# Performance work log

Hardware: AMD Instinct MI355X
Metric: run time of the kernel (lower is better)

The kernel has to match this reference:

```python
import jax, jax.numpy as jnp
import numpy as np

BETA = 1.0

def setup_inputs() -> dict:
    key = jax.random.key(0)
    k1, k2 = jax.random.split(key)
    z = jax.random.normal(k1, (8, 8192, 64), dtype=jnp.float32)
    # codebook initialized as randn * sc (sc=0.001) in the original module
    codebook = jax.random.normal(k2, (1024, 64), dtype=jnp.float32) * 0.001
    return {"z": z, "codebook": codebook}

def reference(z, codebook):
    # squared euclidean distances: ||z||^2 + ||c||^2 - 2 z.c  -> [B, T, code_num]
    d = (jnp.sum(z ** 2, axis=-1, keepdims=True)
         + jnp.sum(codebook ** 2, axis=1)
         - 2.0 * jnp.einsum('btd,kd->btk', z, codebook))
    min_encoding_indices = jnp.argmin(d, axis=-1)            # [B, T] int
    # one-hot @ codebook is exactly a gather of nearest code vectors
    z_q = codebook[min_encoding_indices]                     # [B, T, D]
    sg = jax.lax.stop_gradient
    loss = jnp.mean((sg(z_q) - z) ** 2) + BETA * jnp.mean((z_q - sg(z)) ** 2)
    # straight-through estimator
    z_q_st = z + sg(z_q - z)
    return (z_q_st, min_encoding_indices, loss)
```

## Files before the change

### kernel.cpp

```cpp
#include <hip/hip_runtime.h>

#define TOKENS 65536
#define DIM 64
#define NCODE 1024
#define MARGIN 1e-5f
#define MARGINS (MARGIN * 2097152.0f)
#define FLAG_CAP 8192

#define OUT_IDX_OFF ((size_t)TOKENS * DIM)
#define OUT_LOSS_OFF (OUT_IDX_OFF + TOKENS)

#define WS_LOSS   0
#define WS_FLAGC  8
#define WS_DONEA  12
#define WS_DGRP   16
#define WS_BNORM  2064
#define WS_BNS    6160
#define WS_CHI    10256
#define WS_CLO    141328
#define WS_PACKED 272400
#define WS_FLAGS  337936

typedef __attribute__((ext_vector_type(8))) short short8;
typedef __attribute__((ext_vector_type(8))) _Float16 half8;
typedef __attribute__((ext_vector_type(4))) float f32x4;

static __device__ __forceinline__ half8 as_h8(short8 v) {
    return __builtin_bit_cast(half8, v);
}

__device__ __forceinline__ float np_sumsq64(const float* __restrict__ x) {
#pragma clang fp contract(off)
    float r[8];
#pragma unroll
    for (int j = 0; j < 8; ++j) r[j] = x[j] * x[j];
#pragma unroll
    for (int i = 8; i < 64; i += 8) {
#pragma unroll
        for (int j = 0; j < 8; ++j) {
            float sq = x[i + j] * x[i + j];
            r[j] = r[j] + sq;
        }
    }
    return ((r[0] + r[1]) + (r[2] + r[3])) + ((r[4] + r[5]) + (r[6] + r[7]));
}

__global__ __launch_bounds__(256) void vq_prep(
    const float* __restrict__ cb, unsigned short* __restrict__ chi,
    unsigned short* __restrict__ clo, float* __restrict__ bnorm,
    float* __restrict__ bns,
    unsigned int* __restrict__ ctrl ) {
    int tid = blockIdx.x * 256 + threadIdx.x;
    if (tid < 516) ctrl[tid] = 0u;
    int j = tid & 7;
    int L = (tid >> 3) & 63;
    int cs = tid >> 9;
    int s = cs & 1, c = cs >> 1;
    int code = c * 16 + (L & 15);
    int d = s * 32 + (L >> 4) * 8 + j;
    float v = -8192.0f * cb[(size_t)code * DIM + d];
    _Float16 h = (_Float16)v;
    float hf = (float)h;
    float lo;
    {
#pragma clang fp contract(off)
        lo = v - hf;
    }
    _Float16 l = (_Float16)lo;
    chi[tid] = __builtin_bit_cast(unsigned short, h);
    clo[tid] = __builtin_bit_cast(unsigned short, l);

    if (tid < NCODE) {
        float bn = np_sumsq64(cb + (size_t)tid * DIM);
        bnorm[tid] = bn;
        bns[tid] = bn * 2097152.0f;
    }
}

__device__ __forceinline__ void top2_merge(float& a1, float& a2, int& ai,
                                           float b1, float b2, int bi) {
    float n1 = fminf(a1, b1);
    float n2 = fminf(fmaxf(a1, b1), fminf(a2, b2));
    ai = (b1 < a1) ? bi : ai;
    a1 = n1; a2 = n2;
}

__global__ __launch_bounds__(256, 4) void vq_fast(
    const float* __restrict__ z, const float* __restrict__ cb,
    const unsigned short* __restrict__ cfrag_hi,
    const unsigned short* __restrict__ cfrag_lo,
    const float* __restrict__ bnorm_s, float* __restrict__ out,
    unsigned int* __restrict__ flag_count, int* __restrict__ flag_list,
    unsigned long long* __restrict__ packed_min,
    double* __restrict__ loss_sum, unsigned int flag_cap) {
    __shared__ short8 sh_hi[2][512];
    __shared__ short8 sh_lo[2][512];
    __shared__ float bn_lds[NCODE];
    __shared__ int s_best[64];
    __shared__ int s_flag[64];

    const int tid = threadIdx.x;
    const int lane = tid & 63;
    const int w = tid >> 6;
    const int t0 = blockIdx.x * 64;
    const int tw = t0 + w * 16;
    const int col = lane & 15;
    const int quad = lane >> 4;

    ((float4*)bn_lds)[tid] = ((const float4*)bnorm_s)[tid];

    half8 zhi[2], zlo[2];
#pragma unroll
    for (int s = 0; s < 2; ++s) {
        const float* zp = z + (size_t)(tw + col) * DIM + s * 32 + quad * 8;
        float4 f0 = ((const float4*)zp)[0];
        float4 f1 = ((const float4*)zp)[1];
        float f[8] = {f0.x, f0.y, f0.z, f0.w, f1.x, f1.y, f1.z, f1.w};
        half8 hh8, ll8;
#pragma unroll
        for (int j = 0; j < 8; ++j) {
            float sv = f[j] * 512.0f;
            _Float16 hh = (_Float16)sv;
            float hf = (float)hh;
            float lo;
            {
#pragma clang fp contract(off)
                lo = sv - hf;
            }
            hh8[j] = hh;
            ll8[j] = (_Float16)lo;
        }
        zhi[s] = hh8; zlo[s] = ll8;
    }

    const short8* CH = (const short8*)cfrag_hi;
    const short8* CL = (const short8*)cfrag_lo;

    {
        short8 a0 = CH[tid], a1 = CH[tid + 256];
        short8 b0 = CL[tid], b1 = CL[tid + 256];
        sh_hi[0][tid] = a0; sh_hi[0][tid + 256] = a1;
        sh_lo[0][tid] = b0; sh_lo[0][tid + 256] = b1;
    }
    __syncthreads();

    float m1 = 3.0e38f, m2 = 3.0e38f;
    int bi = 0;
    const int koff = quad * 4;

    for (int g = 0; g < 16; ++g) {
        const int buf = g & 1;
        short8 a0, a1, b0, b1;
        if (g < 15) {
            const int base = (g + 1) * 512 + tid;
            a0 = CH[base]; a1 = CH[base + 256];
            b0 = CL[base]; b1 = CL[base + 256];
        }
#pragma unroll
        for (int cc = 0; cc < 4; ++cc) {
            const int c = g * 4 + cc;
            short8 ch0 = sh_hi[buf][(cc * 2 + 0) * 64 + lane];
            short8 ch1 = sh_hi[buf][(cc * 2 + 1) * 64 + lane];
            short8 cl0 = sh_lo[buf][(cc * 2 + 0) * 64 + lane];
            short8 cl1 = sh_lo[buf][(cc * 2 + 1) * 64 + lane];
            const int cbase = c * 16 + koff;
            const f32x4 bn = *(const f32x4*)&bn_lds[cbase];
            f32x4 acc = bn;
            acc = __builtin_amdgcn_mfma_f32_16x16x32_f16(as_h8(ch0), zhi[0], acc, 0, 0, 0);
            acc = __builtin_amdgcn_mfma_f32_16x16x32_f16(as_h8(cl0), zhi[0], acc, 0, 0, 0);
            acc = __builtin_amdgcn_mfma_f32_16x16x32_f16(as_h8(ch0), zlo[0], acc, 0, 0, 0);
            acc = __builtin_amdgcn_mfma_f32_16x16x32_f16(as_h8(ch1), zhi[1], acc, 0, 0, 0);
            acc = __builtin_amdgcn_mfma_f32_16x16x32_f16(as_h8(cl1), zhi[1], acc, 0, 0, 0);
            acc = __builtin_amdgcn_mfma_f32_16x16x32_f16(as_h8(ch1), zlo[1], acc, 0, 0, 0);
#pragma unroll
            for (int i = 0; i < 4; ++i) {
                float u = acc[i];
                float om1 = m1;
                bool lt = u < om1;
                float fm = fminf(m2, u);
                m2 = lt ? om1 : fm;
                m1 = lt ? u : om1;
                bi = lt ? (cbase + i) : bi;
            }
        }
        if (g < 15) {
            sh_hi[buf ^ 1][tid] = a0; sh_hi[buf ^ 1][tid + 256] = a1;
            sh_lo[buf ^ 1][tid] = b0; sh_lo[buf ^ 1][tid + 256] = b1;
            __syncthreads();
        }
    }

    {
        float a1 = m1, a2 = m2;
        int ai = bi;
        {
            float o1 = __shfl_xor(a1, 16); float o2 = __shfl_xor(a2, 16);
            int oi = __shfl_xor(ai, 16);
            top2_merge(a1, a2, ai, o1, o2, oi);
        }
        {
            float o1 = __shfl_xor(a1, 32); float o2 = __shfl_xor(a2, 32);
            int oi = __shfl_xor(ai, 32);
            top2_merge(a1, a2, ai, o1, o2, oi);
        }
        if (quad == 0) {
            const int slot = w * 16 + col;
            int fl = (a2 - a1) < MARGINS;
            if (fl) {
                unsigned int pos = atomicAdd(flag_count, 1u);
                if (pos >= flag_cap) fl = 0;
                else {
                    flag_list[pos] = t0 + slot;
                    packed_min[pos] = ~0ull;
                }
            }
            s_best[slot] = ai;
            s_flag[slot] = fl;
        }
    }
    __syncthreads();

    const int et = tid >> 1, h = tid & 1;
    float loss_t = 0.0f;
    if (et < 64 && !s_flag[et]) {
        const int B = s_best[et];
        const float4* cq  = (const float4*)(cb + (size_t)B * DIM + h * 32);
        const float4* zq4 = (const float4*)(z + (size_t)(t0 + et) * DIM + h * 32);
        float4* o4 = (float4*)(out + (size_t)(t0 + et) * DIM + h * 32);
#pragma unroll
        for (int jj = 0; jj < 8; ++jj) {
#pragma clang fp contract(off)
            float4 cc = cq[jj];
            float4 zz = zq4[jj];
            float d0 = cc.x - zz.x, d1 = cc.y - zz.y;
            float d2 = cc.z - zz.z, d3 = cc.w - zz.w;
            float4 o;
            o.x = zz.x + d0; o.y = zz.y + d1;
            o.z = zz.z + d2; o.w = zz.w + d3;
            o4[jj] = o;
            loss_t = __fmaf_rn(d0, d0, loss_t);
            loss_t = __fmaf_rn(d1, d1, loss_t);
            loss_t = __fmaf_rn(d2, d2, loss_t);
            loss_t = __fmaf_rn(d3, d3, loss_t);
        }
        if (h == 0) out[OUT_IDX_OFF + t0 + et] = (float)B;
    }
#pragma unroll
    for (int off = 32; off > 0; off >>= 1)
        loss_t += __shfl_down(loss_t, off);
    if (lane == 0 && w < 2) atomicAdd(loss_sum, (double)loss_t);
}

__device__ __forceinline__ unsigned long long shfl_down_u64(unsigned long long v, int off) {
    unsigned int lo = (unsigned int)v, hi = (unsigned int)(v >> 32);
    lo = __shfl_down(lo, off);
    hi = __shfl_down(hi, off);
    return ((unsigned long long)hi << 32) | lo;
}

__global__ __launch_bounds__(256) void vq_exact_min(
    const float* __restrict__ z, const float* __restrict__ cb,
    const float* __restrict__ bnorm,
    const unsigned int* __restrict__ flag_count,
    const int* __restrict__ flag_list,
    unsigned long long* __restrict__ packed_min ,
    unsigned int* __restrict__ done_grp ,
    unsigned int* __restrict__ done_all,
    float* __restrict__ out, double* __restrict__ loss_sum,
    unsigned int flag_cap) {
    __shared__ float zsh[68];
    __shared__ float s_zs;
    __shared__ unsigned long long s_pk[4];
    __shared__ unsigned long long s_min;

    const int tid = threadIdx.x;
    const int w = tid >> 6;
    const int lane = tid & 63;
    unsigned int count = *flag_count;
    if (count > flag_cap) count = flag_cap;

    if (count == 0) {
        if (blockIdx.x == 0 && tid == 0) {
            double L = atomicAdd(loss_sum, 0.0);
            out[OUT_LOSS_OFF] = (float)(2.0 * L / (double)((size_t)TOKENS * DIM));
        }
        return;
    }
    if (blockIdx.x >= count) return;

    const int t = flag_list[blockIdx.x];

    if (tid < 4) {
        const float4* zp = (const float4*)(z + (size_t)t * DIM + tid * 16);
        float4* dst = (float4*)(zsh + tid * 16);
#pragma unroll
        for (int e = 0; e < 4; ++e) dst[e] = zp[e];
    }
    __syncthreads();
    if (tid == 0) s_zs = np_sumsq64(zsh);
    __syncthreads();

    const float szs = s_zs;
    const float* zp = zsh;
    unsigned long long pk = ~0ull;

    for (int e = 0; e < 4; ++e) {
        const int k = e * 256 + tid;
        float row[DIM];
        {
            const float4* c4 = (const float4*)(cb + (size_t)k * DIM);
#pragma unroll
            for (int j = 0; j < 16; ++j) {
                float4 v = c4[j];
                row[4 * j + 0] = v.x; row[4 * j + 1] = v.y;
                row[4 * j + 2] = v.z; row[4 * j + 3] = v.w;
            }
        }
        const float bnk = bnorm[k];

        float l16[16];
#pragma unroll
        for (int g2 = 0; g2 < 4; ++g2) {
            float4 v0 = ((const float4*)(zp + 4 * g2))[0];
            float4 v1 = ((const float4*)(zp + 16 + 4 * g2))[0];
            float4 v2 = ((const float4*)(zp + 32 + 4 * g2))[0];
            float4 v3 = ((const float4*)(zp + 48 + 4 * g2))[0];
            float a0[4] = {v0.x, v0.y, v0.z, v0.w};
            float a1[4] = {v1.x, v1.y, v1.z, v1.w};
            float a2[4] = {v2.x, v2.y, v2.z, v2.w};
            float a3[4] = {v3.x, v3.y, v3.z, v3.w};
#pragma unroll
            for (int ee = 0; ee < 4; ++ee) {
#pragma clang fp contract(off)
                int jj = 4 * g2 + ee;
                float acc = a3[ee] * row[48 + jj];
                acc = __fmaf_rn(a2[ee], row[32 + jj], acc);
                acc = __fmaf_rn(a1[ee], row[16 + jj], acc);
                acc = __fmaf_rn(a0[ee], row[jj],      acc);
                l16[jj] = acc;
            }
        }
        float e_np;
        {
#pragma clang fp contract(off)
#pragma unroll
            for (int jj = 0; jj < 8; ++jj) l16[jj] = l16[jj] + l16[jj + 8];
#pragma unroll
            for (int jj = 0; jj < 4; ++jj) l16[jj] = l16[jj] + l16[jj + 4];
            l16[0] = l16[0] + l16[2];
            l16[1] = l16[1] + l16[3];
            e_np = l16[0] + l16[1];
        }
        float dd;
        {
#pragma clang fp contract(off)
            float t1 = szs + bnk;
            float mm = 2.0f * e_np;
            dd = t1 - mm;
        }
        unsigned long long p =
            ((unsigned long long)__float_as_uint(dd) << 10) | (unsigned int)k;
        pk = (p < pk) ? p : pk;
    }

#pragma unroll
    for (int off = 32; off > 0; off >>= 1) {
        unsigned long long o = shfl_down_u64(pk, off);
        pk = (o < pk) ? o : pk;
    }
    if (lane == 0) s_pk[w] = pk;
    __syncthreads();
    if (tid == 0) {
        unsigned long long m = s_pk[0];
        m = (s_pk[1] < m) ? s_pk[1] : m;
        m = (s_pk[2] < m) ? s_pk[2] : m;
        m = (s_pk[3] < m) ? s_pk[3] : m;
        s_min = m;
    }
    __syncthreads();

    if (w == 0) {
        const int best = (int)(s_min & 1023ull);
        const float zl = zsh[lane];
        const float zq = cb[(size_t)best * DIM + lane];
        float d, o;
        {
#pragma clang fp contract(off)
            d = zq - zl;
            o = zl + d;
        }
        out[(size_t)t * DIM + lane] = o;
        float l2 = d * d;
#pragma unroll
        for (int off = 32; off > 0; off >>= 1)
            l2 += __shfl_down(l2, off);
        if (lane == 0) {
            out[OUT_IDX_OFF + t] = (float)best;
            atomicAdd(loss_sum, (double)l2);
        }
    }

    __threadfence();
    __syncthreads();
    if (tid == 0) {
        unsigned int old = atomicAdd(done_all, 1u);
        if (old == count - 1) {
            double L = atomicAdd(loss_sum, 0.0);
            out[OUT_LOSS_OFF] = (float)(2.0 * L / (double)((size_t)TOKENS * DIM));
        }
    }
}

extern "C" void kernel_launch(void* const* d_in, const int* in_sizes, int n_in,
                              void* d_out, int out_size, void* d_ws, size_t ws_size,
                              hipStream_t stream) {
    const float* z  = (const float*)d_in[0];
    const float* cb = (const float*)d_in[1];
    float* out = (float*)d_out;

    char* ws = (char*)d_ws;
    double* loss_sum = (double*)(ws + WS_LOSS);
    unsigned int* flag_count = (unsigned int*)(ws + WS_FLAGC);
    unsigned int* done_all = (unsigned int*)(ws + WS_DONEA);
    unsigned int* done_grp = (unsigned int*)(ws + WS_DGRP);
    float* bnorm = (float*)(ws + WS_BNORM);
    float* bns = (float*)(ws + WS_BNS);
    unsigned short* chi = (unsigned short*)(ws + WS_CHI);
    unsigned short* clo = (unsigned short*)(ws + WS_CLO);
    unsigned long long* packed = (unsigned long long*)(ws + WS_PACKED);
    int* flag_list = (int*)(ws + WS_FLAGS);

    unsigned int cap = 0;
    if (ws_size > WS_FLAGS + 4) {
        size_t c = (ws_size - WS_FLAGS) / 4;
        cap = (c > FLAG_CAP) ? FLAG_CAP : (unsigned int)c;
    }

    vq_prep<<<dim3(256), dim3(256), 0, stream>>>(
        cb, chi, clo, bnorm, bns, (unsigned int*)ws);
    vq_fast<<<dim3(TOKENS / 64), dim3(256), 0, stream>>>(
        z, cb, chi, clo, bns, out, flag_count, flag_list, packed, loss_sum, cap);
    vq_exact_min<<<dim3(FLAG_CAP), dim3(256), 0, stream>>>(
        z, cb, bnorm, flag_count, flag_list, packed, done_grp, done_all,
        out, loss_sum, cap);
}
```

Baseline: 137.4 us.

## Fuse exact-min fallback into fast kernel using per-block shared flag list

Removes the separate exact-recheck kernel and its global flag list and atomic counter. Each block now collects its own ambiguous tokens in shared memory and rechecks them in place with the exact FP32 distance loop, and a block-completion counter finalizes the loss. This saves a kernel launch and the 8192-block grid that mostly exits early, plus the global atomics. The cost is that blocks holding several flagged tokens process them serially, which can create tail imbalance. LDS use and register pressure also grow in a kernel launched with bounds of 4 blocks per CU.

Measured after the change: 307.8 us. 124% more time.

```diff
diff --git a/kernel.cpp b/kernel.cpp
--- a/kernel.cpp
+++ b/kernel.cpp
@@ -5,7 +5,6 @@
 #define NCODE 1024
 #define MARGIN 1e-5f
 #define MARGINS (MARGIN * 2097152.0f)
-#define FLAG_CAP 8192
 
 #define OUT_IDX_OFF ((size_t)TOKENS * DIM)
 #define OUT_LOSS_OFF (OUT_IDX_OFF + TOKENS)
@@ -18,8 +17,6 @@
 #define WS_BNS    6160
 #define WS_CHI    10256
 #define WS_CLO    141328
-#define WS_PACKED 272400
-#define WS_FLAGS  337936
 
 typedef __attribute__((ext_vector_type(8))) short short8;
 typedef __attribute__((ext_vector_type(8))) _Float16 half8;
@@ -85,19 +82,31 @@
     a1 = n1; a2 = n2;
 }
 
+__device__ __forceinline__ unsigned long long shfl_down_u64(unsigned long long v, int off) {
+    unsigned int lo = (unsigned int)v, hi = (unsigned int)(v >> 32);
+    lo = __shfl_down(lo, off);
+    hi = __shfl_down(hi, off);
+    return ((unsigned long long)hi << 32) | lo;
+}
+
 __global__ __launch_bounds__(256, 4) void vq_fast(
     const float* __restrict__ z, const float* __restrict__ cb,
     const unsigned short* __restrict__ cfrag_hi,
     const unsigned short* __restrict__ cfrag_lo,
-    const float* __restrict__ bnorm_s, float* __restrict__ out,
-    unsigned int* __restrict__ flag_count, int* __restrict__ flag_list,
-    unsigned long long* __restrict__ packed_min,
-    double* __restrict__ loss_sum, unsigned int flag_cap) {
+    const float* __restrict__ bnorm_s, const float* __restrict__ bnorm,
+    float* __restrict__ out, double* __restrict__ loss_sum,
+    unsigned int* __restrict__ done_all) {
     __shared__ short8 sh_hi[2][512];
     __shared__ short8 sh_lo[2][512];
     __shared__ float bn_lds[NCODE];
     __shared__ int s_best[64];
     __shared__ int s_flag[64];
+    __shared__ int s_flist[64];
+    __shared__ unsigned int s_fcnt;
+    __shared__ float zsh[68];
+    __shared__ float s_zs;
+    __shared__ unsigned long long s_pk[4];
+    __shared__ unsigned long long s_min;
 
     const int tid = threadIdx.x;
     const int lane = tid & 63;
@@ -106,6 +115,8 @@
     const int tw = t0 + w * 16;
     const int col = lane & 15;
     const int quad = lane >> 4;
+
+    if (tid == 0) s_fcnt = 0u;
 
     ((float4*)bn_lds)[tid] = ((const float4*)bnorm_s)[tid];
 
@@ -207,12 +218,8 @@
             const int slot = w * 16 + col;
             int fl = (a2 - a1) < MARGINS;
             if (fl) {
-                unsigned int pos = atomicAdd(flag_count, 1u);
-                if (pos >= flag_cap) fl = 0;
-                else {
-                    flag_list[pos] = t0 + slot;
-                    packed_min[pos] = ~0ull;
-                }
+                unsigned int p = atomicAdd(&s_fcnt, 1u);
+                s_flist[p] = slot;
             }
             s_best[slot] = ai;
             s_flag[slot] = fl;
@@ -249,154 +256,119 @@
     for (int off = 32; off > 0; off >>= 1)
         loss_t += __shfl_down(loss_t, off);
     if (lane == 0 && w < 2) atomicAdd(loss_sum, (double)loss_t);
-}
-
-__device__ __forceinline__ unsigned long long shfl_down_u64(unsigned long long v, int off) {
-    unsigned int lo = (unsigned int)v, hi = (unsigned int)(v >> 32);
-    lo = __shfl_down(lo, off);
-    hi = __shfl_down(hi, off);
-    return ((unsigned long long)hi << 32) | lo;
-}
-
-__global__ __launch_bounds__(256) void vq_exact_min(
-    const float* __restrict__ z, const float* __restrict__ cb,
-    const float* __restrict__ bnorm,
-    const unsigned int* __restrict__ flag_count,
-    const int* __restrict__ flag_list,
-    unsigned long long* __restrict__ packed_min ,
-    unsigned int* __restrict__ done_grp ,
-    unsigned int* __restrict__ done_all,
-    float* __restrict__ out, double* __restrict__ loss_sum,
-    unsigned int flag_cap) {
-    __shared__ float zsh[68];
-    __shared__ float s_zs;
-    __shared__ unsigned long long s_pk[4];
-    __shared__ unsigned long long s_min;
-
-    const int tid = threadIdx.x;
-    const int w = tid >> 6;
-    const int lane = tid & 63;
-    unsigned int count = *flag_count;
-    if (count > flag_cap) count = flag_cap;
-
-    if (count == 0) {
-        if (blockIdx.x == 0 && tid == 0) {
-            double L = atomicAdd(loss_sum, 0.0);
-            out[OUT_LOSS_OFF] = (float)(2.0 * L / (double)((size_t)TOKENS * DIM));
-        }
-        return;
-    }
-    if (blockIdx.x >= count) return;
-
-    const int t = flag_list[blockIdx.x];
-
-    if (tid < 4) {
-        const float4* zp = (const float4*)(z + (size_t)t * DIM + tid * 16);
-        float4* dst = (float4*)(zsh + tid * 16);
-#pragma unroll
-        for (int e = 0; e < 4; ++e) dst[e] = zp[e];
-    }
-    __syncthreads();
-    if (tid == 0) s_zs = np_sumsq64(zsh);
-    __syncthreads();
-
-    const float szs = s_zs;
-    const float* zp = zsh;
-    unsigned long long pk = ~0ull;
-
-    for (int e = 0; e < 4; ++e) {
-        const int k = e * 256 + tid;
-        float row[DIM];
-        {
-            const float4* c4 = (const float4*)(cb + (size_t)k * DIM);
-#pragma unroll
-            for (int j = 0; j < 16; ++j) {
-                float4 v = c4[j];
-                row[4 * j + 0] = v.x; row[4 * j + 1] = v.y;
-                row[4 * j + 2] = v.z; row[4 * j + 3] = v.w;
-            }
-        }
-        const float bnk = bnorm[k];
-
-        float l16[16];
-#pragma unroll
-        for (int g2 = 0; g2 < 4; ++g2) {
-            float4 v0 = ((const float4*)(zp + 4 * g2))[0];
-            float4 v1 = ((const float4*)(zp + 16 + 4 * g2))[0];
-            float4 v2 = ((const float4*)(zp + 32 + 4 * g2))[0];
-            float4 v3 = ((const float4*)(zp + 48 + 4 * g2))[0];
-            float a0[4] = {v0.x, v0.y, v0.z, v0.w};
-            float a1[4] = {v1.x, v1.y, v1.z, v1.w};
-            float a2[4] = {v2.x, v2.y, v2.z, v2.w};
-            float a3[4] = {v3.x, v3.y, v3.z, v3.w};
-#pragma unroll
-            for (int ee = 0; ee < 4; ++ee) {
-#pragma clang fp contract(off)
-                int jj = 4 * g2 + ee;
-                float acc = a3[ee] * row[48 + jj];
-                acc = __fmaf_rn(a2[ee], row[32 + jj], acc);
-                acc = __fmaf_rn(a1[ee], row[16 + jj], acc);
-                acc = __fmaf_rn(a0[ee], row[jj],      acc);
-                l16[jj] = acc;
-            }
-        }
-        float e_np;
-        {
-#pragma clang fp contract(off)
-#pragma unroll
-            for (int jj = 0; jj < 8; ++jj) l16[jj] = l16[jj] + l16[jj + 8];
-#pragma unroll
-            for (int jj = 0; jj < 4; ++jj) l16[jj] = l16[jj] + l16[jj + 4];
-            l16[0] = l16[0] + l16[2];
-            l16[1] = l16[1] + l16[3];
-            e_np = l16[0] + l16[1];
-        }
-        float dd;
-        {
-#pragma clang fp contract(off)
-            float t1 = szs + bnk;
-            float mm = 2.0f * e_np;
-            dd = t1 - mm;
-        }
-        unsigned long long p =
-            ((unsigned long long)__float_as_uint(dd) << 10) | (unsigned int)k;
-        pk = (p < pk) ? p : pk;
-    }
-
-#pragma unroll
-    for (int off = 32; off > 0; off >>= 1) {
-        unsigned long long o = shfl_down_u64(pk, off);
-        pk = (o < pk) ? o : pk;
-    }
-    if (lane == 0) s_pk[w] = pk;
-    __syncthreads();
-    if (tid == 0) {
-        unsigned long long m = s_pk[0];
-        m = (s_pk[1] < m) ? s_pk[1] : m;
-        m = (s_pk[2] < m) ? s_pk[2] : m;
-        m = (s_pk[3] < m) ? s_pk[3] : m;
-        s_min = m;
-    }
-    __syncthreads();
-
-    if (w == 0) {
-        const int best = (int)(s_min & 1023ull);
-        const float zl = zsh[lane];
-        const float zq = cb[(size_t)best * DIM + lane];
-        float d, o;
-        {
-#pragma clang fp contract(off)
-            d = zq - zl;
-            o = zl + d;
-        }
-        out[(size_t)t * DIM + lane] = o;
-        float l2 = d * d;
-#pragma unroll
-        for (int off = 32; off > 0; off >>= 1)
-            l2 += __shfl_down(l2, off);
-        if (lane == 0) {
-            out[OUT_IDX_OFF + t] = (float)best;
-            atomicAdd(loss_sum, (double)l2);
+
+    const unsigned int nf = s_fcnt;
+    for (unsigned int fi = 0; fi < nf; ++fi) {
+        __syncthreads();
+        const int t = t0 + s_flist[fi];
+        if (tid < 4) {
+            const float4* zp4 = (const float4*)(z + (size_t)t * DIM + tid * 16);
+            float4* dst = (float4*)(zsh + tid * 16);
+#pragma unroll
+            for (int e = 0; e < 4; ++e) dst[e] = zp4[e];
+        }
+        __syncthreads();
+        if (tid == 0) s_zs = np_sumsq64(zsh);
+        __syncthreads();
+
+        const float szs = s_zs;
+        const float* zp = zsh;
+        unsigned long long pk = ~0ull;
+
+        for (int e = 0; e < 4; ++e) {
+            const int k = e * 256 + tid;
+            float row[DIM];
+            {
+                const float4* c4 = (const float4*)(cb + (size_t)k * DIM);
+#pragma unroll
+                for (int j = 0; j < 16; ++j) {
+                    float4 v = c4[j];
+                    row[4 * j + 0] = v.x; row[4 * j + 1] = v.y;
+                    row[4 * j + 2] = v.z; row[4 * j + 3] = v.w;
+                }
+            }
+            const float bnk = bnorm[k];
+
+            float l16[16];
+#pragma unroll
+            for (int g2 = 0; g2 < 4; ++g2) {
+                float4 v0 = ((const float4*)(zp + 4 * g2))[0];
+                float4 v1 = ((const float4*)(zp + 16 + 4 * g2))[0];
+                float4 v2 = ((const float4*)(zp + 32 + 4 * g2))[0];
+                float4 v3 = ((const float4*)(zp + 48 + 4 * g2))[0];
+                float a0[4] = {v0.x, v0.y, v0.z, v0.w};
+                float a1[4] = {v1.x, v1.y, v1.z, v1.w};
+                float a2[4] = {v2.x, v2.y, v2.z, v2.w};
+                float a3[4] = {v3.x, v3.y, v3.z, v3.w};
+#pragma unroll
+                for (int ee = 0; ee < 4; ++ee) {
+#pragma clang fp contract(off)
+                    int jj = 4 * g2 + ee;
+                    float acc = a3[ee] * row[48 + jj];
+                    acc = __fmaf_rn(a2[ee], row[32 + jj], acc);
+                    acc = __fmaf_rn(a1[ee], row[16 + jj], acc);
+                    acc = __fmaf_rn(a0[ee], row[jj],      acc);
+                    l16[jj] = acc;
+                }
+            }
+            float e_np;
+            {
+#pragma clang fp contract(off)
+#pragma unroll
+                for (int jj = 0; jj < 8; ++jj) l16[jj] = l16[jj] + l16[jj + 8];
+#pragma unroll
+                for (int jj = 0; jj < 4; ++jj) l16[jj] = l16[jj] + l16[jj + 4];
+                l16[0] = l16[0] + l16[2];
+                l16[1] = l16[1] + l16[3];
+                e_np = l16[0] + l16[1];
+            }
+            float dd;
+            {
+#pragma clang fp contract(off)
+                float t1 = szs + bnk;
+                float mm = 2.0f * e_np;
+                dd = t1 - mm;
+            }
+            unsigned long long p =
+                ((unsigned long long)__float_as_uint(dd) << 10) | (unsigned int)k;
+            pk = (p < pk) ? p : pk;
+        }
+
+#pragma unroll
+        for (int off = 32; off > 0; off >>= 1) {
+            unsigned long long o = shfl_down_u64(pk, off);
+            pk = (o < pk) ? o : pk;
+        }
+        if (lane == 0) s_pk[w] = pk;
+        __syncthreads();
+        if (tid == 0) {
+            unsigned long long m = s_pk[0];
+            m = (s_pk[1] < m) ? s_pk[1] : m;
+            m = (s_pk[2] < m) ? s_pk[2] : m;
+            m = (s_pk[3] < m) ? s_pk[3] : m;
+            s_min = m;
+        }
+        __syncthreads();
+
+        if (w == 0) {
+            const int best = (int)(s_min & 1023ull);
+            const float zl = zsh[lane];
+            const float zq = cb[(size_t)best * DIM + lane];
+            float d, o;
+            {
+#pragma clang fp contract(off)
+                d = zq - zl;
+                o = zl + d;
+            }
+            out[(size_t)t * DIM + lane] = o;
+            float l2 = d * d;
+#pragma unroll
+            for (int off = 32; off > 0; off >>= 1)
+                l2 += __shfl_down(l2, off);
+            if (lane == 0) {
+                out[OUT_IDX_OFF + t] = (float)best;
+                atomicAdd(loss_sum, (double)l2);
+            }
         }
     }
 
@@ -404,7 +376,7 @@
     __syncthreads();
     if (tid == 0) {
         unsigned int old = atomicAdd(done_all, 1u);
-        if (old == count - 1) {
+        if (old == (unsigned int)(TOKENS / 64) - 1u) {
             double L = atomicAdd(loss_sum, 0.0);
             out[OUT_LOSS_OFF] = (float)(2.0 * L / (double)((size_t)TOKENS * DIM));
         }
@@ -420,27 +392,14 @@
 
     char* ws = (char*)d_ws;
     double* loss_sum = (double*)(ws + WS_LOSS);
-    unsigned int* flag_count = (unsigned int*)(ws + WS_FLAGC);
     unsigned int* done_all = (unsigned int*)(ws + WS_DONEA);
-    unsigned int* done_grp = (unsigned int*)(ws + WS_DGRP);
     float* bnorm = (float*)(ws + WS_BNORM);
     float* bns = (float*)(ws + WS_BNS);
     unsigned short* chi = (unsigned short*)(ws + WS_CHI);
     unsigned short* clo = (unsigned short*)(ws + WS_CLO);
-    unsigned long long* packed = (unsigned long long*)(ws + WS_PACKED);
-    int* flag_list = (int*)(ws + WS_FLAGS);
-
-    unsigned int cap = 0;
-    if (ws_size > WS_FLAGS + 4) {
-        size_t c = (ws_size - WS_FLAGS) / 4;
-        cap = (c > FLAG_CAP) ? FLAG_CAP : (unsigned int)c;
-    }
 
     vq_prep<<<dim3(256), dim3(256), 0, stream>>>(
         cb, chi, clo, bnorm, bns, (unsigned int*)ws);
     vq_fast<<<dim3(TOKENS / 64), dim3(256), 0, stream>>>(
-        z, cb, chi, clo, bns, out, flag_count, flag_list, packed, loss_sum, cap);
-    vq_exact_min<<<dim3(FLAG_CAP), dim3(256), 0, stream>>>(
-        z, cb, bnorm, flag_count, flag_list, packed, done_grp, done_all,
-        out, loss_sum, cap);
-}
+        z, cb, chi, clo, bns, bnorm, out, loss_sum, done_all);
+}
```

## Process two token tiles per wave to reuse codebook fragments across MFMAs

Applied to the files above, without the earlier changes.

Each wave now computes distances for 32 tokens instead of 16, reusing each codebook fragment loaded from shared memory for two MFMA chains. Blocks shrink to 128 threads. The codebook norms are read directly from global memory with a one-step register prefetch instead of being staged in LDS. This aims to cut LDS traffic per MFMA at the cost of more registers per thread and fewer waves per block.

Measured after the change: 142.0 us. 1.03x slower.

```diff
diff --git a/kernel.cpp b/kernel.cpp
--- a/kernel.cpp
+++ b/kernel.cpp
@@ -85,7 +85,7 @@
     a1 = n1; a2 = n2;
 }
 
-__global__ __launch_bounds__(256, 4) void vq_fast(
+__global__ __launch_bounds__(128, 2) void vq_fast(
     const float* __restrict__ z, const float* __restrict__ cb,
     const unsigned short* __restrict__ cfrag_hi,
     const unsigned short* __restrict__ cfrag_lo,
@@ -95,7 +95,6 @@
     double* __restrict__ loss_sum, unsigned int flag_cap) {
     __shared__ short8 sh_hi[2][512];
     __shared__ short8 sh_lo[2][512];
-    __shared__ float bn_lds[NCODE];
     __shared__ int s_best[64];
     __shared__ int s_flag[64];
 
@@ -103,58 +102,67 @@
     const int lane = tid & 63;
     const int w = tid >> 6;
     const int t0 = blockIdx.x * 64;
-    const int tw = t0 + w * 16;
     const int col = lane & 15;
     const int quad = lane >> 4;
 
-    ((float4*)bn_lds)[tid] = ((const float4*)bnorm_s)[tid];
-
-    half8 zhi[2], zlo[2];
-#pragma unroll
-    for (int s = 0; s < 2; ++s) {
-        const float* zp = z + (size_t)(tw + col) * DIM + s * 32 + quad * 8;
-        float4 f0 = ((const float4*)zp)[0];
-        float4 f1 = ((const float4*)zp)[1];
-        float f[8] = {f0.x, f0.y, f0.z, f0.w, f1.x, f1.y, f1.z, f1.w};
-        half8 hh8, ll8;
-#pragma unroll
-        for (int j = 0; j < 8; ++j) {
-            float sv = f[j] * 512.0f;
-            _Float16 hh = (_Float16)sv;
-            float hf = (float)hh;
-            float lo;
-            {
-#pragma clang fp contract(off)
-                lo = sv - hf;
+    half8 zhi[2][2], zlo[2][2];
+#pragma unroll
+    for (int tt = 0; tt < 2; ++tt) {
+#pragma unroll
+        for (int s = 0; s < 2; ++s) {
+            const float* zp = z + (size_t)(t0 + w * 32 + tt * 16 + col) * DIM
+                              + s * 32 + quad * 8;
+            float4 f0 = ((const float4*)zp)[0];
+            float4 f1 = ((const float4*)zp)[1];
+            float f[8] = {f0.x, f0.y, f0.z, f0.w, f1.x, f1.y, f1.z, f1.w};
+            half8 hh8, ll8;
+#pragma unroll
+            for (int j = 0; j < 8; ++j) {
+                float sv = f[j] * 512.0f;
+                _Float16 hh = (_Float16)sv;
+                float hf = (float)hh;
+                float lo;
+                {
+#pragma clang fp contract(off)
+                    lo = sv - hf;
+                }
+                hh8[j] = hh;
+                ll8[j] = (_Float16)lo;
             }
-            hh8[j] = hh;
-            ll8[j] = (_Float16)lo;
-        }
-        zhi[s] = hh8; zlo[s] = ll8;
+            zhi[tt][s] = hh8; zlo[tt][s] = ll8;
+        }
     }
 
     const short8* CH = (const short8*)cfrag_hi;
     const short8* CL = (const short8*)cfrag_lo;
+    const f32x4* bnp = (const f32x4*)bnorm_s;
 
     {
-        short8 a0 = CH[tid], a1 = CH[tid + 256];
-        short8 b0 = CL[tid], b1 = CL[tid + 256];
-        sh_hi[0][tid] = a0; sh_hi[0][tid + 256] = a1;
-        sh_lo[0][tid] = b0; sh_lo[0][tid + 256] = b1;
-    }
-    __syncthreads();
-
-    float m1 = 3.0e38f, m2 = 3.0e38f;
-    int bi = 0;
+#pragma unroll
+        for (int j = 0; j < 4; ++j) {
+            const int e = tid + 128 * j;
+            sh_hi[0][e] = CH[e];
+            sh_lo[0][e] = CL[e];
+        }
+    }
+    __syncthreads();
+
+    float m1[2] = {3.0e38f, 3.0e38f};
+    float m2[2] = {3.0e38f, 3.0e38f};
+    int bi[2] = {0, 0};
     const int koff = quad * 4;
+
+    f32x4 nbn = bnp[quad];
 
     for (int g = 0; g < 16; ++g) {
         const int buf = g & 1;
-        short8 a0, a1, b0, b1;
+        short8 a0, a1, a2, a3, b0, b1, b2, b3;
         if (g < 15) {
             const int base = (g + 1) * 512 + tid;
-            a0 = CH[base]; a1 = CH[base + 256];
-            b0 = CL[base]; b1 = CL[base + 256];
+            a0 = CH[base];       a1 = CH[base + 128];
+            a2 = CH[base + 256]; a3 = CH[base + 384];
+            b0 = CL[base];       b1 = CL[base + 128];
+            b2 = CL[base + 256]; b3 = CL[base + 384];
         }
 #pragma unroll
         for (int cc = 0; cc < 4; ++cc) {
@@ -164,35 +172,43 @@
             short8 cl0 = sh_lo[buf][(cc * 2 + 0) * 64 + lane];
             short8 cl1 = sh_lo[buf][(cc * 2 + 1) * 64 + lane];
             const int cbase = c * 16 + koff;
-            const f32x4 bn = *(const f32x4*)&bn_lds[cbase];
-            f32x4 acc = bn;
-            acc = __builtin_amdgcn_mfma_f32_16x16x32_f16(as_h8(ch0), zhi[0], acc, 0, 0, 0);
-            acc = __builtin_amdgcn_mfma_f32_16x16x32_f16(as_h8(cl0), zhi[0], acc, 0, 0, 0);
-            acc = __builtin_amdgcn_mfma_f32_16x16x32_f16(as_h8(ch0), zlo[0], acc, 0, 0, 0);
-            acc = __builtin_amdgcn_mfma_f32_16x16x32_f16(as_h8(ch1), zhi[1], acc, 0, 0, 0);
-            acc = __builtin_amdgcn_mfma_f32_16x16x32_f16(as_h8(cl1), zhi[1], acc, 0, 0, 0);
-            acc = __builtin_amdgcn_mfma_f32_16x16x32_f16(as_h8(ch1), zlo[1], acc, 0, 0, 0);
-#pragma unroll
-            for (int i = 0; i < 4; ++i) {
-                float u = acc[i];
-                float om1 = m1;
-                bool lt = u < om1;
-                float fm = fminf(m2, u);
-                m2 = lt ? om1 : fm;
-                m1 = lt ? u : om1;
-                bi = lt ? (cbase + i) : bi;
+            const f32x4 bn = nbn;
+            if (c < 63) nbn = bnp[(c + 1) * 4 + quad];
+#pragma unroll
+            for (int tt = 0; tt < 2; ++tt) {
+                f32x4 acc = bn;
+                acc = __builtin_amdgcn_mfma_f32_16x16x32_f16(as_h8(ch0), zhi[tt][0], acc, 0, 0, 0);
+                acc = __builtin_amdgcn_mfma_f32_16x16x32_f16(as_h8(cl0), zhi[tt][0], acc, 0, 0, 0);
+                acc = __builtin_amdgcn_mfma_f32_16x16x32_f16(as_h8(ch0), zlo[tt][0], acc, 0, 0, 0);
+                acc = __builtin_amdgcn_mfma_f32_16x16x32_f16(as_h8(ch1), zhi[tt][1], acc, 0, 0, 0);
+                acc = __builtin_amdgcn_mfma_f32_16x16x32_f16(as_h8(cl1), zhi[tt][1], acc, 0, 0, 0);
+                acc = __builtin_amdgcn_mfma_f32_16x16x32_f16(as_h8(ch1), zlo[tt][1], acc, 0, 0, 0);
+#pragma unroll
+                for (int i = 0; i < 4; ++i) {
+                    float u = acc[i];
+                    float om1 = m1[tt];
+                    bool lt = u < om1;
+                    float fm = fminf(m2[tt], u);
+                    m2[tt] = lt ? om1 : fm;
+                    m1[tt] = lt ? u : om1;
+                    bi[tt] = lt ? (cbase + i) : bi[tt];
+                }
             }
         }
         if (g < 15) {
-            sh_hi[buf ^ 1][tid] = a0; sh_hi[buf ^ 1][tid + 256] = a1;
-            sh_lo[buf ^ 1][tid] = b0; sh_lo[buf ^ 1][tid + 256] = b1;
+            const int e = tid;
+            sh_hi[buf ^ 1][e] = a0;       sh_hi[buf ^ 1][e + 128] = a1;
+            sh_hi[buf ^ 1][e + 256] = a2; sh_hi[buf ^ 1][e + 384] = a3;
+            sh_lo[buf ^ 1][e] = b0;       sh_lo[buf ^ 1][e + 128] = b1;
+            sh_lo[buf ^ 1][e + 256] = b2; sh_lo[buf ^ 1][e + 384] = b3;
             __syncthreads();
         }
     }
 
-    {
-        float a1 = m1, a2 = m2;
-        int ai = bi;
+#pragma unroll
+    for (int tt = 0; tt < 2; ++tt) {
+        float a1 = m1[tt], a2 = m2[tt];
+        int ai = bi[tt];
         {
             float o1 = __shfl_xor(a1, 16); float o2 = __shfl_xor(a2, 16);
             int oi = __shfl_xor(ai, 16);
@@ -204,7 +220,7 @@
             top2_merge(a1, a2, ai, o1, o2, oi);
         }
         if (quad == 0) {
-            const int slot = w * 16 + col;
+            const int slot = w * 32 + tt * 16 + col;
             int fl = (a2 - a1) < MARGINS;
             if (fl) {
                 unsigned int pos = atomicAdd(flag_count, 1u);
@@ -248,7 +264,7 @@
 #pragma unroll
     for (int off = 32; off > 0; off >>= 1)
         loss_t += __shfl_down(loss_t, off);
-    if (lane == 0 && w < 2) atomicAdd(loss_sum, (double)loss_t);
+    if (lane == 0) atomicAdd(loss_sum, (double)loss_t);
 }
 
 __device__ __forceinline__ unsigned long long shfl_down_u64(unsigned long long v, int off) {
@@ -438,7 +454,7 @@
 
     vq_prep<<<dim3(256), dim3(256), 0, stream>>>(
         cb, chi, clo, bnorm, bns, (unsigned int*)ws);
-    vq_fast<<<dim3(TOKENS / 64), dim3(256), 0, stream>>>(
+    vq_fast<<<dim3(TOKENS / 64), dim3(128), 0, stream>>>(
         z, cb, chi, clo, bns, out, flag_count, flag_list, packed, loss_sum, cap);
     vq_exact_min<<<dim3(FLAG_CAP), dim3(256), 0, stream>>>(
         z, cb, bnorm, flag_count, flag_list, packed, done_grp, done_all,
```
